# Kernel optimization log

Measured on AMD Instinct MI355X. Metric: run time of the kernel, lower is better.

The kernel has to match this reference:

```python
import jax, jax.numpy as jnp
import numpy as np

B, E, N, F = 8, 2048, 2048, 128

def setup_inputs() -> dict:
    key = jax.random.key(0)
    k1, k2, k3, k4 = jax.random.split(key, 4)
    node_embeddings = jax.random.normal(k1, (B, N, F), dtype=jnp.float32)
    adj = jax.random.randint(k2, (B, E, N), -1, 3).astype(jnp.float32)
    W = jax.random.normal(k3, (F, F), dtype=jnp.float32) * (1.0 / np.sqrt(F))
    b = jax.random.normal(k4, (F,), dtype=jnp.float32) * 0.01
    return {"node_embeddings": node_embeddings, "adj": adj, "W": W, "b": b}

def reference(node_embeddings, adj, W, b):
    # adj_target: 1 where adj == -1, else 0
    adj_target = (adj == -1).astype(node_embeddings.dtype)          # [B, E, N]
    norm = jnp.sum(adj_target, axis=-1, keepdims=True)               # [B, E, 1]
    norm = jnp.where(norm == 0, 1.0, norm)
    # masked-mean aggregation of neighbor vertices into hyperedges
    message_vertex = jnp.matmul(adj_target, node_embeddings) / norm  # [B, E, F]
    # linear (torch Linear: x @ W.T + b) + relu
    hyperedge_embeddings = jax.nn.relu(jnp.matmul(message_vertex, W.T) + b)
    return hyperedge_embeddings
```

## Files before the change

kernel.cpp:

```cpp
#include <hip/hip_runtime.h>
#include <hip/hip_bf16.h>

#define B_ 8
#define E_ 2048
#define N_ 2048
#define F_ 128

#define BM 16
#define BK 64
#define MP 136

using bf16x8 = __bf16 __attribute__((ext_vector_type(8)));
using fx4    = float __attribute__((ext_vector_type(4)));

__global__ __launch_bounds__(256) void prep_node(const float* __restrict__ node,
                                                 __bf16* __restrict__ nodeT) {
    const int bid = blockIdx.x;
    const int b   = bid & 7;
    const int n0  = (bid >> 3) * 32;
    const int t   = threadIdx.x;
    const int f   = t & 127;
    const int nb  = n0 + (t >> 7) * 16;

    const float* src = node + ((size_t)b * N_ + nb) * F_ + f;
    __bf16 h[16];
#pragma unroll
    for (int i = 0; i < 16; ++i)
        h[i] = (__bf16)src[(size_t)i * F_];

    __bf16* dst = nodeT + ((size_t)b * F_ + f) * N_ + nb;
    *(uint4*)&dst[0] = *(const uint4*)&h[0];
    *(uint4*)&dst[8] = *(const uint4*)&h[8];
}

__global__ __launch_bounds__(256) void prep_w(const float* __restrict__ W,
                                              __bf16* __restrict__ Wb) {
    int idx = blockIdx.x * 256 + threadIdx.x;
    float4 v = *(const float4*)&W[idx * 4];
    __bf16 o[4] = {(__bf16)v.x, (__bf16)v.y, (__bf16)v.z, (__bf16)v.w};
    *(uint2*)&Wb[idx * 4] = *(const uint2*)o;
}

__global__ __launch_bounds__(256, 4) void v2h_main(const float* __restrict__ adj,
                                                   const __bf16* __restrict__ nodeT,
                                                   const __bf16* __restrict__ Wb,
                                                   const float* __restrict__ bias,
                                                   float* __restrict__ out) {
    __shared__ __align__(16) __bf16 Bs[2][128][64];
    __shared__ __align__(16) __bf16 Ms[BM * MP];

    const int t    = threadIdx.x;
    const int bid  = blockIdx.x;
    const int b    = bid & 7;
    const int e0   = (bid >> 3) * BM;
    const int w    = t >> 6;
    const int lane = t & 63;
    const int l15  = lane & 15;
    const int quad = lane >> 4;

    const float*  aRow = adj + ((size_t)b * E_ + e0 + l15) * N_ + quad * 8;
    const __bf16* nTB  = nodeT + (size_t)b * F_ * N_;

    auto issue_dma = [&](int k0, int buf) {
#pragma unroll
        for (int p = 0; p < 4; ++p) {
            int idx = t + 256 * p;
            int f   = idx >> 3;
            int sl  = idx & 7;
            int g   = sl ^ (f & 7);
            const __bf16* src = nTB + (size_t)f * N_ + k0 + g * 8;
            __bf16* dst = &Bs[buf][0][0] + (size_t)(w * 64 + 256 * p) * 8;
            __builtin_amdgcn_global_load_lds(
                (const __attribute__((address_space(1))) void*)src,
                (__attribute__((address_space(3))) void*)dst, 16, 0, 0);
        }
    };

    fx4 acc[2] = {};
    float cnt = 0.f;

    issue_dma(0, 0);
    float4 aR0 = *(const float4*)(aRow + 0);
    float4 aR1 = *(const float4*)(aRow + 4);
    float4 aR2 = *(const float4*)(aRow + 32);
    float4 aR3 = *(const float4*)(aRow + 36);

    for (int k0 = 0; k0 < N_; k0 += BK) {
        const int buf = (k0 >> 6) & 1;
        __syncthreads();

        const int kn = (k0 + BK) & (N_ - 1);
        issue_dma(kn, buf ^ 1);
        float4 aN0 = *(const float4*)(aRow + kn);
        float4 aN1 = *(const float4*)(aRow + kn + 4);
        float4 aN2 = *(const float4*)(aRow + kn + 32);
        float4 aN3 = *(const float4*)(aRow + kn + 36);

        bf16x8 af[2];
        {
            float m0 = (aR0.x == -1.f) ? 1.f : 0.f;
            float m1 = (aR0.y == -1.f) ? 1.f : 0.f;
            float m2 = (aR0.z == -1.f) ? 1.f : 0.f;
            float m3 = (aR0.w == -1.f) ? 1.f : 0.f;
            float m4 = (aR1.x == -1.f) ? 1.f : 0.f;
            float m5 = (aR1.y == -1.f) ? 1.f : 0.f;
            float m6 = (aR1.z == -1.f) ? 1.f : 0.f;
            float m7 = (aR1.w == -1.f) ? 1.f : 0.f;
            cnt += (m0 + m1) + (m2 + m3) + ((m4 + m5) + (m6 + m7));
            af[0][0] = (__bf16)m0; af[0][1] = (__bf16)m1; af[0][2] = (__bf16)m2; af[0][3] = (__bf16)m3;
            af[0][4] = (__bf16)m4; af[0][5] = (__bf16)m5; af[0][6] = (__bf16)m6; af[0][7] = (__bf16)m7;
        }
        {
            float m0 = (aR2.x == -1.f) ? 1.f : 0.f;
            float m1 = (aR2.y == -1.f) ? 1.f : 0.f;
            float m2 = (aR2.z == -1.f) ? 1.f : 0.f;
            float m3 = (aR2.w == -1.f) ? 1.f : 0.f;
            float m4 = (aR3.x == -1.f) ? 1.f : 0.f;
            float m5 = (aR3.y == -1.f) ? 1.f : 0.f;
            float m6 = (aR3.z == -1.f) ? 1.f : 0.f;
            float m7 = (aR3.w == -1.f) ? 1.f : 0.f;
            cnt += (m0 + m1) + (m2 + m3) + ((m4 + m5) + (m6 + m7));
            af[1][0] = (__bf16)m0; af[1][1] = (__bf16)m1; af[1][2] = (__bf16)m2; af[1][3] = (__bf16)m3;
            af[1][4] = (__bf16)m4; af[1][5] = (__bf16)m5; af[1][6] = (__bf16)m6; af[1][7] = (__bf16)m7;
        }

#pragma unroll
        for (int ks = 0; ks < 2; ++ks) {
#pragma unroll
            for (int ft = 0; ft < 2; ++ft) {
                int f = w * 32 + ft * 16 + l15;
                int q = ks * 4 + quad;
                bf16x8 bfr = *(const bf16x8*)&Bs[buf][f][(q ^ (f & 7)) * 8];
                acc[ft] = __builtin_amdgcn_mfma_f32_16x16x32_bf16(af[ks], bfr, acc[ft], 0, 0, 0);
            }
        }

        aR0 = aN0; aR1 = aN1; aR2 = aN2; aR3 = aN3;
    }

    cnt += __shfl_xor(cnt, 16);
    cnt += __shfl_xor(cnt, 32);

    const int rbase = quad * 4;
    float rn[4];
#pragma unroll
    for (int r = 0; r < 4; ++r)
        rn[r] = 1.f / fmaxf(__shfl(cnt, rbase + r), 1.f);

#pragma unroll
    for (int ft = 0; ft < 2; ++ft) {
        int fcol = w * 32 + ft * 16 + l15;
#pragma unroll
        for (int r = 0; r < 4; ++r)
            Ms[(rbase + r) * MP + fcol] = (__bf16)(acc[ft][r] * rn[r]);
    }
    __syncthreads();

    fx4 acc2[2] = {};
#pragma unroll
    for (int ks = 0; ks < 4; ++ks) {
        bf16x8 afm = *(const bf16x8*)&Ms[l15 * MP + ks * 32 + quad * 8];
#pragma unroll
        for (int gt = 0; gt < 2; ++gt) {
            int g = w * 32 + gt * 16 + l15;
            bf16x8 wfr = *(const bf16x8*)&Wb[(size_t)g * F_ + ks * 32 + quad * 8];
            acc2[gt] = __builtin_amdgcn_mfma_f32_16x16x32_bf16(afm, wfr, acc2[gt], 0, 0, 0);
        }
    }

#pragma unroll
    for (int gt = 0; gt < 2; ++gt) {
        int g = w * 32 + gt * 16 + l15;
        float bb = bias[g];
#pragma unroll
        for (int r = 0; r < 4; ++r) {
            int e = e0 + rbase + r;
            float v = acc2[gt][r] + bb;
            out[((size_t)b * E_ + e) * F_ + g] = fmaxf(v, 0.f);
        }
    }
}

extern "C" void kernel_launch(void* const* d_in, const int* in_sizes, int n_in,
                              void* d_out, int out_size, void* d_ws, size_t ws_size,
                              hipStream_t stream) {
    const float* node = (const float*)d_in[0];
    const float* adj  = (const float*)d_in[1];
    const float* W    = (const float*)d_in[2];
    const float* bias = (const float*)d_in[3];
    float* out = (float*)d_out;

    __bf16* nodeT = (__bf16*)d_ws;
    __bf16* Wb    = (__bf16*)((char*)d_ws + (size_t)B_ * F_ * N_ * 2);

    prep_node<<<512, 256, 0, stream>>>(node, nodeT);
    prep_w<<<16, 256, 0, stream>>>(W, Wb);
    v2h_main<<<1024, 256, 0, stream>>>(adj, nodeT, Wb, bias, out);
}
```

Measured before the change: 252.6 us.

## Pre-pack adjacency sentinel mask into bitfields in a separate kernel

Adds a prep_adj kernel that reads each adjacency row once, packs the ==-1 test into bits laid out in MFMA fragment order, and writes a per-row reciprocal count. The main kernel then loads the whole per-lane bitmask up front and unpacks bytes into bf16 fragments. This removes the strided fp32 adjacency loads and per-element compares from the MFMA loop, so that loop only streams node tiles. The cost is an extra kernel launch and a second full pass over adj (still ~134MB read), plus a small intermediate buffer.

```diff
diff --git a/kernel.cpp b/kernel.cpp
--- a/kernel.cpp
+++ b/kernel.cpp
@@ -41,10 +41,53 @@
     *(uint2*)&Wb[idx * 4] = *(const uint2*)o;
 }
 
-__global__ __launch_bounds__(256, 4) void v2h_main(const float* __restrict__ adj,
+__global__ __launch_bounds__(256) void prep_adj(const float* __restrict__ adj,
+                                                unsigned char* __restrict__ bitsT,
+                                                float* __restrict__ rcount) {
+    __shared__ __align__(16) unsigned char rowB[256];
+    __shared__ float cw[4];
+    const int row = blockIdx.x;
+    const int t   = threadIdx.x;
+
+    const float* src = adj + (size_t)row * N_ + t * 8;
+    float4 v0 = *(const float4*)src;
+    float4 v1 = *(const float4*)(src + 4);
+    unsigned m = 0;
+    m |= (v0.x == -1.f) ? 1u   : 0u;
+    m |= (v0.y == -1.f) ? 2u   : 0u;
+    m |= (v0.z == -1.f) ? 4u   : 0u;
+    m |= (v0.w == -1.f) ? 8u   : 0u;
+    m |= (v1.x == -1.f) ? 16u  : 0u;
+    m |= (v1.y == -1.f) ? 32u  : 0u;
+    m |= (v1.z == -1.f) ? 64u  : 0u;
+    m |= (v1.w == -1.f) ? 128u : 0u;
+
+    const int q  = t & 3;
+    const int ks = (t >> 2) & 1;
+    const int mm = t >> 3;
+    rowB[q * 64 + mm * 2 + ks] = (unsigned char)m;
+
+    float c = (float)__popc(m);
+#pragma unroll
+    for (int s = 1; s < 64; s <<= 1) c += __shfl_xor(c, s);
+    if ((t & 63) == 0) cw[t >> 6] = c;
+    __syncthreads();
+
+    if (t < 64) {
+        unsigned d = *(const unsigned*)&rowB[t * 4];
+        *(unsigned*)&bitsT[(size_t)row * 256 + t * 4] = d;
+    }
+    if (t == 0) {
+        float tot = cw[0] + cw[1] + cw[2] + cw[3];
+        rcount[row] = 1.f / fmaxf(tot, 1.f);
+    }
+}
+
+__global__ __launch_bounds__(256, 4) void v2h_main(const unsigned char* __restrict__ bitsT,
                                                    const __bf16* __restrict__ nodeT,
                                                    const __bf16* __restrict__ Wb,
                                                    const float* __restrict__ bias,
+                                                   const float* __restrict__ rcount,
                                                    float* __restrict__ out) {
     __shared__ __align__(16) __bf16 Bs[2][128][64];
     __shared__ __align__(16) __bf16 Ms[BM * MP];
@@ -58,8 +101,7 @@
     const int l15  = lane & 15;
     const int quad = lane >> 4;
 
-    const float*  aRow = adj + ((size_t)b * E_ + e0 + l15) * N_ + quad * 8;
-    const __bf16* nTB  = nodeT + (size_t)b * F_ * N_;
+    const __bf16* nTB = nodeT + (size_t)b * F_ * N_;
 
     auto issue_dma = [&](int k0, int buf) {
 #pragma unroll
@@ -76,77 +118,56 @@
         }
     };
 
+    const unsigned char* rbP = bitsT + ((size_t)b * E_ + e0 + l15) * 256 + quad * 64;
+    uint4 rb0 = *(const uint4*)(rbP +  0);
+    uint4 rb1 = *(const uint4*)(rbP + 16);
+    uint4 rb2 = *(const uint4*)(rbP + 32);
+    uint4 rb3 = *(const uint4*)(rbP + 48);
+    unsigned rw[16] = {rb0.x, rb0.y, rb0.z, rb0.w, rb1.x, rb1.y, rb1.z, rb1.w,
+                       rb2.x, rb2.y, rb2.z, rb2.w, rb3.x, rb3.y, rb3.z, rb3.w};
+
+    auto unpack = [](unsigned byte) -> bf16x8 {
+        union { unsigned u[4]; bf16x8 v; } r;
+        r.u[0] = ((byte &   1u) ? 0x3F80u : 0u) | ((byte &   2u) ? 0x3F800000u : 0u);
+        r.u[1] = ((byte &   4u) ? 0x3F80u : 0u) | ((byte &   8u) ? 0x3F800000u : 0u);
+        r.u[2] = ((byte &  16u) ? 0x3F80u : 0u) | ((byte &  32u) ? 0x3F800000u : 0u);
+        r.u[3] = ((byte &  64u) ? 0x3F80u : 0u) | ((byte & 128u) ? 0x3F800000u : 0u);
+        return r.v;
+    };
+
     fx4 acc[2] = {};
-    float cnt = 0.f;
 
     issue_dma(0, 0);
-    float4 aR0 = *(const float4*)(aRow + 0);
-    float4 aR1 = *(const float4*)(aRow + 4);
-    float4 aR2 = *(const float4*)(aRow + 32);
-    float4 aR3 = *(const float4*)(aRow + 36);
-
-    for (int k0 = 0; k0 < N_; k0 += BK) {
-        const int buf = (k0 >> 6) & 1;
+
+#pragma unroll
+    for (int m = 0; m < 32; ++m) {
+        const int buf = m & 1;
         __syncthreads();
 
-        const int kn = (k0 + BK) & (N_ - 1);
-        issue_dma(kn, buf ^ 1);
-        float4 aN0 = *(const float4*)(aRow + kn);
-        float4 aN1 = *(const float4*)(aRow + kn + 4);
-        float4 aN2 = *(const float4*)(aRow + kn + 32);
-        float4 aN3 = *(const float4*)(aRow + kn + 36);
-
-        bf16x8 af[2];
-        {
-            float m0 = (aR0.x == -1.f) ? 1.f : 0.f;
-            float m1 = (aR0.y == -1.f) ? 1.f : 0.f;
-            float m2 = (aR0.z == -1.f) ? 1.f : 0.f;
-            float m3 = (aR0.w == -1.f) ? 1.f : 0.f;
-            float m4 = (aR1.x == -1.f) ? 1.f : 0.f;
-            float m5 = (aR1.y == -1.f) ? 1.f : 0.f;
-            float m6 = (aR1.z == -1.f) ? 1.f : 0.f;
-            float m7 = (aR1.w == -1.f) ? 1.f : 0.f;
-            cnt += (m0 + m1) + (m2 + m3) + ((m4 + m5) + (m6 + m7));
-            af[0][0] = (__bf16)m0; af[0][1] = (__bf16)m1; af[0][2] = (__bf16)m2; af[0][3] = (__bf16)m3;
-            af[0][4] = (__bf16)m4; af[0][5] = (__bf16)m5; af[0][6] = (__bf16)m6; af[0][7] = (__bf16)m7;
-        }
-        {
-            float m0 = (aR2.x == -1.f) ? 1.f : 0.f;
-            float m1 = (aR2.y == -1.f) ? 1.f : 0.f;
-            float m2 = (aR2.z == -1.f) ? 1.f : 0.f;
-            float m3 = (aR2.w == -1.f) ? 1.f : 0.f;
-            float m4 = (aR3.x == -1.f) ? 1.f : 0.f;
-            float m5 = (aR3.y == -1.f) ? 1.f : 0.f;
-            float m6 = (aR3.z == -1.f) ? 1.f : 0.f;
-            float m7 = (aR3.w == -1.f) ? 1.f : 0.f;
-            cnt += (m0 + m1) + (m2 + m3) + ((m4 + m5) + (m6 + m7));
-            af[1][0] = (__bf16)m0; af[1][1] = (__bf16)m1; af[1][2] = (__bf16)m2; af[1][3] = (__bf16)m3;
-            af[1][4] = (__bf16)m4; af[1][5] = (__bf16)m5; af[1][6] = (__bf16)m6; af[1][7] = (__bf16)m7;
-        }
-
-#pragma unroll
-        for (int ks = 0; ks < 2; ++ks) {
-#pragma unroll
-            for (int ft = 0; ft < 2; ++ft) {
-                int f = w * 32 + ft * 16 + l15;
-                int q = ks * 4 + quad;
-                bf16x8 bfr = *(const bf16x8*)&Bs[buf][f][(q ^ (f & 7)) * 8];
-                acc[ft] = __builtin_amdgcn_mfma_f32_16x16x32_bf16(af[ks], bfr, acc[ft], 0, 0, 0);
-            }
-        }
-
-        aR0 = aN0; aR1 = aN1; aR2 = aN2; aR3 = aN3;
-    }
-
-    cnt += __shfl_xor(cnt, 16);
-    cnt += __shfl_xor(cnt, 32);
+        issue_dma(((m + 1) & 31) * BK, buf ^ 1);
+
+        const unsigned word = rw[m >> 1];
+        const int sh = 16 * (m & 1);
+        bf16x8 af0 = unpack((word >> sh) & 255u);
+        bf16x8 af1 = unpack((word >> (sh + 8)) & 255u);
+
+#pragma unroll
+        for (int ft = 0; ft < 2; ++ft) {
+            int f  = w * 32 + ft * 16 + l15;
+            int q0 = quad ^ (f & 7);
+            int q1 = (4 + quad) ^ (f & 7);
+            bf16x8 b0 = *(const bf16x8*)&Bs[buf][f][q0 * 8];
+            acc[ft] = __builtin_amdgcn_mfma_f32_16x16x32_bf16(af0, b0, acc[ft], 0, 0, 0);
+            bf16x8 b1 = *(const bf16x8*)&Bs[buf][f][q1 * 8];
+            acc[ft] = __builtin_amdgcn_mfma_f32_16x16x32_bf16(af1, b1, acc[ft], 0, 0, 0);
+        }
+    }
 
     const int rbase = quad * 4;
     float rn[4];
 #pragma unroll
     for (int r = 0; r < 4; ++r)
-        rn[r] = 1.f / fmaxf(__shfl(cnt, rbase + r), 1.f);
-
+        rn[r] = rcount[(size_t)b * E_ + e0 + rbase + r];
 #pragma unroll
     for (int ft = 0; ft < 2; ++ft) {
         int fcol = w * 32 + ft * 16 + l15;
@@ -190,10 +211,14 @@
     const float* bias = (const float*)d_in[3];
     float* out = (float*)d_out;
 
-    __bf16* nodeT = (__bf16*)d_ws;
-    __bf16* Wb    = (__bf16*)((char*)d_ws + (size_t)B_ * F_ * N_ * 2);
+    char* ws = (char*)d_ws;
+    __bf16*        nodeT = (__bf16*)ws;
+    __bf16*        Wb    = (__bf16*)(ws + 8 * 1024 * 1024);
+    unsigned char* bitsT = (unsigned char*)(ws + 8 * 1024 * 1024 + 65536);
+    float*         rcnt  = (float*)(ws + 12 * 1024 * 1024 + 65536);
 
     prep_node<<<512, 256, 0, stream>>>(node, nodeT);
     prep_w<<<16, 256, 0, stream>>>(W, Wb);
-    v2h_main<<<1024, 256, 0, stream>>>(adj, nodeT, Wb, bias, out);
-}
+    prep_adj<<<B_ * E_, 256, 0, stream>>>(adj, bitsT, rcnt);
+    v2h_main<<<1024, 256, 0, stream>>>(bitsT, nodeT, Wb, bias, rcnt, out);
+}
```

Result: faster. 230.6 us (-8.7%).
